# Kernel optimization log

Measured on AMD Instinct MI355X. Metric: run time of the kernel, lower is better.

The kernel has to match this reference:

```python
import jax, jax.numpy as jnp
import numpy as np

D = 1024

def setup_inputs() -> dict:
    key = jax.random.key(0)
    ks = jax.random.split(key, 7)
    s = 1.0 / np.sqrt(D)
    return {
        "x": jax.random.normal(ks[0], (4, 2048, D), dtype=jnp.float32),
        "Wq": jax.random.uniform(ks[1], (D, D), jnp.float32, -s, s),
        "bq": jax.random.uniform(ks[2], (D,), jnp.float32, -s, s),
        "Wk": jax.random.uniform(ks[3], (D, D), jnp.float32, -s, s),
        "bk": jax.random.uniform(ks[4], (D,), jnp.float32, -s, s),
        "Wv": jax.random.uniform(ks[5], (D, D), jnp.float32, -s, s),
        "bv": jax.random.uniform(ks[6], (D,), jnp.float32, -s, s),
    }

def reference(x, Wq, bq, Wk, bk, Wv, bv):
    # x: [B, S, D]
    q = jnp.einsum('bsd,de->bse', x, Wq.T) + bq
    k = jnp.einsum('bsd,de->bse', x, Wk.T) + bk
    v = jnp.einsum('bsd,de->bse', x, Wv.T) + bv
    scale = 1.0 / jnp.sqrt(jnp.float32(x.shape[-1]))
    score = jnp.einsum('bqd,bkd->bqk', q, k) * scale  # [B, S, S]
    attn = jax.nn.softmax(score, axis=-1)
    return jnp.einsum('bqk,bkd->bqd', attn, v)
```

## Files before the change

### kernel.cpp

```cpp
#include <hip/hip_runtime.h>

typedef short shortx8 __attribute__((ext_vector_type(8)));
typedef float floatx4 __attribute__((ext_vector_type(4)));
typedef unsigned short ushortx4 __attribute__((ext_vector_type(4)));
typedef unsigned short ushortx8 __attribute__((ext_vector_type(8)));

typedef __attribute__((address_space(1))) char gchar;
typedef __attribute__((address_space(3))) char lchar;

__device__ __forceinline__ void async16(const void* g, void* l) {
    __builtin_amdgcn_global_load_lds((gchar*)g, (lchar*)l, 16, 0, 0);
}

__device__ __forceinline__ unsigned short f2bf(float f) {
    union { float f; unsigned int u; } v;
    v.f = f;
    unsigned int r = v.u + 0x7fffu + ((v.u >> 16) & 1u);
    return (unsigned short)(r >> 16);
}

__device__ __forceinline__ float bf2f(unsigned short h) {
    union { unsigned int u; float f; } v;
    v.u = ((unsigned int)h) << 16;
    return v.f;
}

template<int JN>
__device__ __forceinline__ void gemm256_mainloop(
        const ushort* __restrict__ Arow, const ushort* __restrict__ Brow,
        int K, ushort* ldsp, floatx4 (&acc)[8][JN])
{
    const int t = threadIdx.x;
    const int w = t >> 6;
    const int lane = t & 63;
    const size_t ldb = (size_t)K * 2;
    constexpr int ABYTES = 32768;
    constexpr int BBYTES = JN * 8192;
    constexpr int BUFB = ABYTES + BBYTES;
    char* l0 = (char*)ldsp;
    const int wst = w << 10;
    const int sc = (((t & 7) ^ ((t >> 4) & 7)) << 4);
    const char* gA = (const char*)Arow + (size_t)(t >> 3) * ldb + sc;
    const char* gB = (const char*)Brow + (size_t)(t >> 3) * ldb + sc;
    const int fr = lane & 15, kq = lane >> 4;
    const int xr = (fr >> 1) & 7;
    const int ck0 = (kq ^ xr) << 4;
    const int ck1 = ((kq + 4) ^ xr) << 4;
    const int wm = w & 1, wn = w >> 1;
    const int abase = (wm * 128 + fr) * 128;
    const int bbase = (wn * (JN * 16) + fr) * 128;

#define STA(buf, kt, R) async16(gA + (size_t)(R) * ldb + (size_t)(kt) * 128, \
                                l0 + (buf) * BUFB + (R) * 128 + wst)
#define STB(buf, kt, R) async16(gB + (size_t)(R) * ldb + (size_t)(kt) * 128, \
                                l0 + (buf) * BUFB + ABYTES + (R) * 128 + wst)
#define LDA4(buf, mb, ck)                                                          \
    a0 = *(const shortx8*)(l0 + (buf) * BUFB + abase + ((mb) + 0) * 2048 + (ck));  \
    a1 = *(const shortx8*)(l0 + (buf) * BUFB + abase + ((mb) + 1) * 2048 + (ck));  \
    a2 = *(const shortx8*)(l0 + (buf) * BUFB + abase + ((mb) + 2) * 2048 + (ck));  \
    a3 = *(const shortx8*)(l0 + (buf) * BUFB + abase + ((mb) + 3) * 2048 + (ck));
#define LDB(buf, ck, dst)                                                          \
    _Pragma("unroll")                                                              \
    for (int n = 0; n < JN; ++n)                                                   \
        dst[n] = *(const shortx8*)(l0 + (buf) * BUFB + ABYTES + bbase + n * 2048 + (ck));
#define PH(MB, BV)                                                                 \
    __builtin_amdgcn_s_setprio(1);                                                 \
    _Pragma("unroll")                                                              \
    for (int n = 0; n < JN; ++n) {                                                 \
        acc[(MB) + 0][n] = __builtin_amdgcn_mfma_f32_16x16x32_bf16(a0, BV[n], acc[(MB) + 0][n], 0, 0, 0); \
        acc[(MB) + 1][n] = __builtin_amdgcn_mfma_f32_16x16x32_bf16(a1, BV[n], acc[(MB) + 1][n], 0, 0, 0); \
        acc[(MB) + 2][n] = __builtin_amdgcn_mfma_f32_16x16x32_bf16(a2, BV[n], acc[(MB) + 2][n], 0, 0, 0); \
        acc[(MB) + 3][n] = __builtin_amdgcn_mfma_f32_16x16x32_bf16(a3, BV[n], acc[(MB) + 3][n], 0, 0, 0); \
    }                                                                              \
    __builtin_amdgcn_s_setprio(0);
#define PH_OPEN()                                                      \
    __builtin_amdgcn_sched_barrier(0);                                 \
    __builtin_amdgcn_s_barrier();                                      \
    asm volatile("s_waitcnt lgkmcnt(0)" ::: "memory");                 \
    __builtin_amdgcn_sched_barrier(0);
#define PH_CLOSE() __builtin_amdgcn_s_barrier();
#define VMW_A()                                                        \
    asm volatile("s_waitcnt vmcnt(%0)" :: "i"(JN + 4) : "memory");     \
    __builtin_amdgcn_s_barrier();                                      \
    __builtin_amdgcn_sched_barrier(0);
#define VMW_B()                                                        \
    asm volatile("s_waitcnt vmcnt(%0)" :: "i"(JN + 2) : "memory");     \
    __builtin_amdgcn_s_barrier();                                      \
    __builtin_amdgcn_sched_barrier(0);

    const int nk = K >> 6;
    const int nit = nk >> 1;

    STA(0, 0, 0); STA(0, 0, 128);
    STB(0, 0, 0); STB(0, 0, 64);
    if (JN >= 3) STB(0, 0, 128);
    if (JN == 4) STB(0, 0, 192);
    STA(0, 0, 64); STA(0, 0, 192);
    STB(1, 1, 0); STB(1, 1, 64);
    if (JN >= 3) STB(1, 1, 128);
    if (JN == 4) STB(1, 1, 192);
    asm volatile("s_waitcnt vmcnt(%0)" :: "i"(JN + 2) : "memory");
    __builtin_amdgcn_s_barrier();
    __builtin_amdgcn_sched_barrier(0);

    shortx8 a0, a1, a2, a3;
    shortx8 b0[JN], b1[JN];

    for (int it = 0; it < nit; ++it) {
        const int T = 2 * it;
        const int T1 = T + 1;
        int T2 = T + 2; if (T2 > nk - 1) T2 = nk - 1;
        int T3 = T + 3; if (T3 > nk - 1) T3 = nk - 1;

        LDA4(0, 0, ck0); LDB(0, ck0, b0);
        STA(1, T1, 0); STA(1, T1, 128);
        PH_OPEN();
        PH(0, b0);
        PH_CLOSE();

        LDA4(0, 0, ck1); LDB(0, ck1, b1);
        STA(1, T1, 64); STA(1, T1, 192);
        PH_OPEN();
        PH(0, b1);
        VMW_A();

        LDA4(0, 4, ck0);
        STB(0, T2, 0); STB(0, T2, 64);
        PH_OPEN();
        PH(4, b0);
        PH_CLOSE();

        LDA4(0, 4, ck1);
        if (JN >= 3) STB(0, T2, 128);
        if (JN == 4) STB(0, T2, 192);
        PH_OPEN();
        PH(4, b1);
        VMW_B();

        LDA4(1, 0, ck0); LDB(1, ck0, b0);
        STA(0, T2, 0); STA(0, T2, 128);
        PH_OPEN();
        PH(0, b0);
        PH_CLOSE();

        LDA4(1, 0, ck1); LDB(1, ck1, b1);
        STA(0, T2, 64); STA(0, T2, 192);
        PH_OPEN();
        PH(0, b1);
        VMW_A();

        LDA4(1, 4, ck0);
        STB(1, T3, 0); STB(1, T3, 64);
        PH_OPEN();
        PH(4, b0);
        PH_CLOSE();

        LDA4(1, 4, ck1);
        if (JN >= 3) STB(1, T3, 128);
        if (JN == 4) STB(1, T3, 192);
        PH_OPEN();
        PH(4, b1);
        VMW_B();
    }
#undef STA
#undef STB
#undef LDA4
#undef LDB
#undef PH
#undef PH_OPEN
#undef PH_CLOSE
#undef VMW_A
#undef VMW_B
}

__global__ __launch_bounds__(512, 2)
void qkv_gemm(const ushort* __restrict__ xb, const ushort* __restrict__ Wb,
              const float* __restrict__ bq, const float* __restrict__ bk,
              const float* __restrict__ bv,
              ushort* __restrict__ Qs, ushort* __restrict__ Ks,
              ushort* __restrict__ Vt) {
    __shared__ __align__(16) ushort lds[57344];
    const int mbase = blockIdx.y * 256;
    const int nglob = blockIdx.x * 192;
    floatx4 acc[8][3];
    const floatx4 zero = {0.0f, 0.0f, 0.0f, 0.0f};
#pragma unroll
    for (int i = 0; i < 8; ++i)
#pragma unroll
        for (int j = 0; j < 3; ++j) acc[i][j] = zero;

    gemm256_mainloop<3>(xb + (size_t)mbase * 1024, Wb + (size_t)nglob * 1024,
                        1024, lds, acc);

    const int t = threadIdx.x, w = t >> 6, lane = t & 63;
    const int wm = w & 1, wn = w >> 1;
    const int r0 = mbase + wm * 128 + (lane >> 4) * 4;
#pragma unroll
    for (int j = 0; j < 3; ++j) {
        const int cj = nglob + wn * 48 + j * 16;
        const int z = cj >> 10;
        const int gc = (cj & 1023) + (lane & 15);
        const float* bias = (z == 0) ? bq : (z == 1) ? bk : bv;
        const float bj = bias[gc];
        if (z == 0) {
#pragma unroll
            for (int i = 0; i < 8; ++i)
#pragma unroll
                for (int r = 0; r < 4; ++r)
                    Qs[(size_t)(r0 + i * 16 + r) * 1024 + gc] =
                        f2bf((acc[i][j][r] + bj) * 0.03125f);
        } else if (z == 1) {
#pragma unroll
            for (int i = 0; i < 8; ++i)
#pragma unroll
                for (int r = 0; r < 4; ++r)
                    Ks[(size_t)(r0 + i * 16 + r) * 1024 + gc] = f2bf(acc[i][j][r] + bj);
        } else {
#pragma unroll
            for (int i = 0; i < 8; ++i)
#pragma unroll
                for (int r = 0; r < 4; ++r) {
                    int gr = r0 + i * 16 + r;
                    Vt[(size_t)(gr >> 11) * (1024 * 2048) + (size_t)gc * 2048 + (gr & 2047)] =
                        f2bf(acc[i][j][r] + bj);
                }
        }
    }
}

__global__ __launch_bounds__(512, 2)
void gemm_bt_bf16(const ushort* __restrict__ A, size_t sAz,
                  const ushort* __restrict__ B, size_t sBz,
                  ushort* __restrict__ C, size_t sCz, int N, int K) {
    __shared__ __align__(16) ushort lds[65536];
    const int mbase = blockIdx.y * 256;
    const int nbase = blockIdx.x * 256;
    const int z = blockIdx.z;
    floatx4 acc[8][4];
    const floatx4 zero = {0.0f, 0.0f, 0.0f, 0.0f};
#pragma unroll
    for (int i = 0; i < 8; ++i)
#pragma unroll
        for (int j = 0; j < 4; ++j) acc[i][j] = zero;

    gemm256_mainloop<4>(A + z * sAz + (size_t)mbase * K,
                        B + z * sBz + (size_t)nbase * K, K, lds, acc);

    const int t = threadIdx.x, w = t >> 6, lane = t & 63;
    const int wm = w & 1, wn = w >> 1;
    const int r0 = mbase + wm * 128 + (lane >> 4) * 4;
    const int c0 = nbase + wn * 64 + (lane & 15);
    ushort* Cz = C + z * sCz;
#pragma unroll
    for (int i = 0; i < 8; ++i)
#pragma unroll
        for (int j = 0; j < 4; ++j)
#pragma unroll
            for (int r = 0; r < 4; ++r)
                Cz[(size_t)(r0 + i * 16 + r) * N + (c0 + j * 16)] = f2bf(acc[i][j][r]);
}

__global__ __launch_bounds__(512, 2)
void gemm_bt_f32(const ushort* __restrict__ A, size_t sAz,
                 const ushort* __restrict__ B, size_t sBz,
                 float* __restrict__ C, size_t sCz, int N, int K) {
    __shared__ __align__(16) ushort lds[49152];
    const int mbase = blockIdx.y * 256;
    const int nbase = blockIdx.x * 128;
    const int z = blockIdx.z;
    floatx4 acc[8][2];
    const floatx4 zero = {0.0f, 0.0f, 0.0f, 0.0f};
#pragma unroll
    for (int i = 0; i < 8; ++i)
#pragma unroll
        for (int j = 0; j < 2; ++j) acc[i][j] = zero;

    gemm256_mainloop<2>(A + z * sAz + (size_t)mbase * K,
                        B + z * sBz + (size_t)nbase * K, K, lds, acc);

    const int t = threadIdx.x, w = t >> 6, lane = t & 63;
    const int wm = w & 1, wn = w >> 1;
    const int r0 = mbase + wm * 128 + (lane >> 4) * 4;
    const int c0 = nbase + wn * 32 + (lane & 15);
    float* Cz = C + z * sCz;
#pragma unroll
    for (int i = 0; i < 8; ++i)
#pragma unroll
        for (int j = 0; j < 2; ++j)
#pragma unroll
            for (int r = 0; r < 4; ++r)
                Cz[(size_t)(r0 + i * 16 + r) * N + (c0 + j * 16)] = acc[i][j][r];
}

__global__ __launch_bounds__(256)
void softmax_rows_bf16(ushort* __restrict__ SP) {
    const int row = blockIdx.x;
    ushortx8* base = (ushortx8*)(SP + (size_t)row * 2048);
    const int t = threadIdx.x;
    const int w = t >> 6, lane = t & 63;
    ushortx8 v = base[t];
    float f[8];
#pragma unroll
    for (int k = 0; k < 8; ++k) f[k] = bf2f(v[k]);
    float m = f[0];
#pragma unroll
    for (int k = 1; k < 8; ++k) m = fmaxf(m, f[k]);
    for (int o = 32; o > 0; o >>= 1) m = fmaxf(m, __shfl_down(m, o));
    __shared__ float red[4];
    if (lane == 0) red[w] = m;
    __syncthreads();
    m = fmaxf(fmaxf(red[0], red[1]), fmaxf(red[2], red[3]));

    float e[8], s = 0.0f;
#pragma unroll
    for (int k = 0; k < 8; ++k) { e[k] = __expf(f[k] - m); s += e[k]; }
    for (int o = 32; o > 0; o >>= 1) s += __shfl_down(s, o);
    __syncthreads();
    if (lane == 0) red[w] = s;
    __syncthreads();
    float inv = 1.0f / (red[0] + red[1] + red[2] + red[3]);

    ushortx8 o;
#pragma unroll
    for (int k = 0; k < 8; ++k) o[k] = f2bf(e[k] * inv);
    base[t] = o;
}

__global__ __launch_bounds__(256)
void cast_bf16_all(const float* __restrict__ x, const float* __restrict__ Wq,
                   const float* __restrict__ Wk, const float* __restrict__ Wv,
                   ushort* __restrict__ dst) {
    const int NX = 2097152;
    const int NW = 262144;
    int i = blockIdx.x * 256 + threadIdx.x;
    const float* src;
    int off;
    if (i < NX)               { src = x;  off = 0; }
    else if (i < NX + NW)     { src = Wq; off = NX; }
    else if (i < NX + 2 * NW) { src = Wk; off = NX + NW; }
    else                      { src = Wv; off = NX + 2 * NW; }
    float4 v = ((const float4*)src)[i - off];
    ushortx4 o = {f2bf(v.x), f2bf(v.y), f2bf(v.z), f2bf(v.w)};
    ((ushortx4*)dst)[i] = o;
}

extern "C" void kernel_launch(void* const* d_in, const int* in_sizes, int n_in,
                              void* d_out, int out_size, void* d_ws, size_t ws_size,
                              hipStream_t stream) {
    const float* x  = (const float*)d_in[0];
    const float* bq = (const float*)d_in[2];
    const float* bk = (const float*)d_in[4];
    const float* bv = (const float*)d_in[6];
    float* out = (float*)d_out;

    const size_t R = 8192;
    const size_t D = 1024;
    const size_t S = 2048;

    const size_t need = (4 * R * D + 3 * D * D + 4 * S * S) * 2;
    if (ws_size < need) return;

    ushort* xb = (ushort*)d_ws;
    ushort* Wb = xb + R * D;
    ushort* Qs = Wb + 3 * D * D;
    ushort* Ks = Qs + R * D;
    ushort* Vt = Ks + R * D;
    ushort* Sb = Vt + R * D;

    cast_bf16_all<<<dim3(11264), dim3(256), 0, stream>>>(
        x, (const float*)d_in[1], (const float*)d_in[3], (const float*)d_in[5], xb);

    qkv_gemm<<<dim3(16, 32), dim3(512), 0, stream>>>(xb, Wb, bq, bk, bv, Qs, Ks, Vt);

    gemm_bt_bf16<<<dim3(8, 8, 4), dim3(512), 0, stream>>>(Qs, S * D, Ks, S * D, Sb, S * S,
                                                          (int)S, (int)D);

    softmax_rows_bf16<<<dim3((unsigned)(4 * S)), dim3(256), 0, stream>>>(Sb);

    gemm_bt_f32<<<dim3(8, 8, 4), dim3(512), 0, stream>>>(Sb, S * S, Vt, D * S, out, S * D,
                                                         (int)D, (int)S);
}
```

Measured before the change: 246.7 us.

## Replace QKV projection mainloop with simpler 128x128 tile single-buffer GEMM

The QKV projection GEMM moves off the software-pipelined 256x192 tile mainloop onto a new, simpler 128x128 tile mainloop. It uses 256 threads, 4x4 MFMA accumulators per wave and a single-buffered LDS stage with two barriers per K step. The grid grows to 24x64 blocks so each block maps to exactly one of Q/K/V, and the epilogue is simplified accordingly. The aim is better occupancy and wave balance for this GEMM, at the cost of losing the load/compute overlap of the pipelined mainloop and getting less data reuse per tile.

```diff
diff --git a/kernel.cpp b/kernel.cpp
--- a/kernel.cpp
+++ b/kernel.cpp
@@ -23,6 +23,66 @@
     union { unsigned int u; float f; } v;
     v.u = ((unsigned int)h) << 16;
     return v.f;
+}
+
+__device__ __forceinline__ void gemm_mainloop(const ushort* __restrict__ Arow,
+                                              const ushort* __restrict__ Brow,
+                                              int K, ushort* As, ushort* Bs,
+                                              floatx4 acc[4][4]) {
+    const int t = threadIdx.x;
+    const int w = t >> 6;
+    const int lane = t & 63;
+    const size_t ldb = (size_t)K * 2;
+    const int frs = lane >> 3;
+    const int kql = (lane & 7) ^ (lane >> 4);
+    const char* gA0 = (const char*)Arow + (size_t)(32 * w + frs) * ldb + (kql << 4);
+    const char* gA1 = (const char*)Arow + (size_t)(32 * w + 8 + frs) * ldb + ((kql ^ 4) << 4);
+    const char* gB0 = (const char*)Brow + (size_t)(32 * w + frs) * ldb + (kql << 4);
+    const char* gB1 = (const char*)Brow + (size_t)(32 * w + 8 + frs) * ldb + ((kql ^ 4) << 4);
+    char* lA = (char*)As + w * 4096;
+    char* lB = (char*)Bs + w * 4096;
+    const int ga0 = (w & 1) * 4;
+    const int gb0 = (w >> 1) * 4;
+    const int fr = lane & 15;
+    const int kq = lane >> 4;
+    const int xr = (fr >> 1) & 7;
+    const int loff0 = fr * 128 + ((kq ^ xr) << 4);
+    const int loff1 = fr * 128 + (((kq + 4) ^ xr) << 4);
+    const int nk = K >> 6;
+    for (int kt = 0; kt < nk; ++kt) {
+        async16(gA0,            lA);
+        async16(gA1,            lA + 1024);
+        async16(gA0 + 16 * ldb, lA + 2048);
+        async16(gA1 + 16 * ldb, lA + 3072);
+        async16(gB0,            lB);
+        async16(gB1,            lB + 1024);
+        async16(gB0 + 16 * ldb, lB + 2048);
+        async16(gB1 + 16 * ldb, lB + 3072);
+        gA0 += 128; gA1 += 128; gB0 += 128; gB1 += 128;
+        __syncthreads();
+        shortx8 a0[4], b0[4], a1[4], b1[4];
+#pragma unroll
+        for (int i = 0; i < 4; ++i) {
+            a0[i] = *(const shortx8*)((const char*)As + (ga0 + i) * 2048 + loff0);
+            a1[i] = *(const shortx8*)((const char*)As + (ga0 + i) * 2048 + loff1);
+        }
+#pragma unroll
+        for (int j = 0; j < 4; ++j) {
+            b0[j] = *(const shortx8*)((const char*)Bs + (gb0 + j) * 2048 + loff0);
+            b1[j] = *(const shortx8*)((const char*)Bs + (gb0 + j) * 2048 + loff1);
+        }
+#pragma unroll
+        for (int i = 0; i < 4; ++i)
+#pragma unroll
+            for (int j = 0; j < 4; ++j)
+                acc[i][j] = __builtin_amdgcn_mfma_f32_16x16x32_bf16(a0[i], b0[j], acc[i][j], 0, 0, 0);
+#pragma unroll
+        for (int i = 0; i < 4; ++i)
+#pragma unroll
+            for (int j = 0; j < 4; ++j)
+                acc[i][j] = __builtin_amdgcn_mfma_f32_16x16x32_bf16(a1[i], b1[j], acc[i][j], 0, 0, 0);
+        __syncthreads();
+    }
 }
 
 template<int JN>
@@ -93,12 +153,10 @@
 
     STA(0, 0, 0); STA(0, 0, 128);
     STB(0, 0, 0); STB(0, 0, 64);
-    if (JN >= 3) STB(0, 0, 128);
-    if (JN == 4) STB(0, 0, 192);
+    if (JN == 4) { STB(0, 0, 128); STB(0, 0, 192); }
     STA(0, 0, 64); STA(0, 0, 192);
     STB(1, 1, 0); STB(1, 1, 64);
-    if (JN >= 3) STB(1, 1, 128);
-    if (JN == 4) STB(1, 1, 192);
+    if (JN == 4) { STB(1, 1, 128); STB(1, 1, 192); }
     asm volatile("s_waitcnt vmcnt(%0)" :: "i"(JN + 2) : "memory");
     __builtin_amdgcn_s_barrier();
     __builtin_amdgcn_sched_barrier(0);
@@ -131,8 +189,7 @@
         PH_CLOSE();
 
         LDA4(0, 4, ck1);
-        if (JN >= 3) STB(0, T2, 128);
-        if (JN == 4) STB(0, T2, 192);
+        if (JN == 4) { STB(0, T2, 128); STB(0, T2, 192); }
         PH_OPEN();
         PH(4, b1);
         VMW_B();
@@ -156,8 +213,7 @@
         PH_CLOSE();
 
         LDA4(1, 4, ck1);
-        if (JN >= 3) STB(1, T3, 128);
-        if (JN == 4) STB(1, T3, 192);
+        if (JN == 4) { STB(1, T3, 128); STB(1, T3, 192); }
         PH_OPEN();
         PH(4, b1);
         VMW_B();
@@ -173,58 +229,61 @@
 #undef VMW_B
 }
 
-__global__ __launch_bounds__(512, 2)
+__global__ __launch_bounds__(256, 3)
 void qkv_gemm(const ushort* __restrict__ xb, const ushort* __restrict__ Wb,
               const float* __restrict__ bq, const float* __restrict__ bk,
               const float* __restrict__ bv,
               ushort* __restrict__ Qs, ushort* __restrict__ Ks,
               ushort* __restrict__ Vt) {
-    __shared__ __align__(16) ushort lds[57344];
-    const int mbase = blockIdx.y * 256;
-    const int nglob = blockIdx.x * 192;
-    floatx4 acc[8][3];
+    __shared__ __align__(16) ushort lds[16384];
+    const int mbase = blockIdx.y * 128;
+    const int nglob = blockIdx.x * 128;
+    const int z = nglob >> 10;
+    const int nbase = nglob & 1023;
+    floatx4 acc[4][4];
     const floatx4 zero = {0.0f, 0.0f, 0.0f, 0.0f};
 #pragma unroll
-    for (int i = 0; i < 8; ++i)
-#pragma unroll
-        for (int j = 0; j < 3; ++j) acc[i][j] = zero;
-
-    gemm256_mainloop<3>(xb + (size_t)mbase * 1024, Wb + (size_t)nglob * 1024,
-                        1024, lds, acc);
+    for (int i = 0; i < 4; ++i)
+#pragma unroll
+        for (int j = 0; j < 4; ++j) acc[i][j] = zero;
+
+    gemm_mainloop(xb + (size_t)mbase * 1024, Wb + (size_t)nglob * 1024,
+                  1024, lds, lds + 8192, acc);
 
     const int t = threadIdx.x, w = t >> 6, lane = t & 63;
-    const int wm = w & 1, wn = w >> 1;
-    const int r0 = mbase + wm * 128 + (lane >> 4) * 4;
-#pragma unroll
-    for (int j = 0; j < 3; ++j) {
-        const int cj = nglob + wn * 48 + j * 16;
-        const int z = cj >> 10;
-        const int gc = (cj & 1023) + (lane & 15);
-        const float* bias = (z == 0) ? bq : (z == 1) ? bk : bv;
-        const float bj = bias[gc];
-        if (z == 0) {
-#pragma unroll
-            for (int i = 0; i < 8; ++i)
-#pragma unroll
-                for (int r = 0; r < 4; ++r)
-                    Qs[(size_t)(r0 + i * 16 + r) * 1024 + gc] =
-                        f2bf((acc[i][j][r] + bj) * 0.03125f);
-        } else if (z == 1) {
-#pragma unroll
-            for (int i = 0; i < 8; ++i)
-#pragma unroll
-                for (int r = 0; r < 4; ++r)
-                    Ks[(size_t)(r0 + i * 16 + r) * 1024 + gc] = f2bf(acc[i][j][r] + bj);
-        } else {
-#pragma unroll
-            for (int i = 0; i < 8; ++i)
+    const int mw = (w & 1) * 64, nw = (w >> 1) * 64;
+    const int r0 = mbase + mw + (lane >> 4) * 4;
+    const int c0 = nbase + nw + (lane & 15);
+    const float* bias = (z == 0) ? bq : (z == 1) ? bk : bv;
+    const float scale = (z == 0) ? 0.03125f : 1.0f;
+    float bj[4];
+#pragma unroll
+    for (int j = 0; j < 4; ++j) bj[j] = bias[c0 + j * 16];
+
+    if (z < 2) {
+        ushort* O = (z == 0) ? Qs : Ks;
+#pragma unroll
+        for (int i = 0; i < 4; ++i)
+#pragma unroll
+            for (int j = 0; j < 4; ++j)
 #pragma unroll
                 for (int r = 0; r < 4; ++r) {
                     int gr = r0 + i * 16 + r;
+                    int gc = c0 + j * 16;
+                    O[(size_t)gr * 1024 + gc] = f2bf((acc[i][j][r] + bj[j]) * scale);
+                }
+    } else {
+#pragma unroll
+        for (int i = 0; i < 4; ++i)
+#pragma unroll
+            for (int j = 0; j < 4; ++j)
+#pragma unroll
+                for (int r = 0; r < 4; ++r) {
+                    int gr = r0 + i * 16 + r;
+                    int gc = c0 + j * 16;
                     Vt[(size_t)(gr >> 11) * (1024 * 2048) + (size_t)gc * 2048 + (gr & 2047)] =
-                        f2bf(acc[i][j][r] + bj);
+                        f2bf(acc[i][j][r] + bj[j]);
                 }
-        }
     }
 }
 
@@ -370,7 +429,7 @@
     cast_bf16_all<<<dim3(11264), dim3(256), 0, stream>>>(
         x, (const float*)d_in[1], (const float*)d_in[3], (const float*)d_in[5], xb);
 
-    qkv_gemm<<<dim3(16, 32), dim3(512), 0, stream>>>(xb, Wb, bq, bk, bv, Qs, Ks, Vt);
+    qkv_gemm<<<dim3(24, 64), dim3(256), 0, stream>>>(xb, Wb, bq, bk, bv, Qs, Ks, Vt);
 
     gemm_bt_bf16<<<dim3(8, 8, 4), dim3(512), 0, stream>>>(Qs, S * D, Ks, S * D, Sb, S * S,
                                                           (int)S, (int)D);
```

Measured after the change: 247.2 us. Within noise of the previous version (+0.2%).
